# Optimization experiments

Measured on AMD Instinct MI355X. Metric: run time of the kernel, lower is better.

The kernel has to match this reference:

```python
import jax, jax.numpy as jnp
import numpy as np
from jax import lax

EPS = 1e-8

def _norm(v, eps=EPS):
    # matches torch F.normalize: v / max(||v||, eps)
    return v / jnp.maximum(jnp.linalg.norm(v, axis=-1, keepdims=True), eps)

def keep_r6(r6):
    v1 = _norm(r6[..., :3])
    v2 = r6[..., 3:6]
    v2 = v2 - jnp.sum(v2 * v1, axis=-1, keepdims=True) * v1
    v2n = jnp.linalg.norm(v2, axis=-1, keepdims=True)
    mask = (v2n < 1e-6).astype(r6.dtype)
    e1 = jnp.array([1.0, 0.0, 0.0], dtype=r6.dtype)
    e2 = jnp.array([0.0, 1.0, 0.0], dtype=r6.dtype)
    dot = jnp.abs(jnp.sum(v1 * e1, axis=-1, keepdims=True))
    fb = jnp.where(dot < 0.9, e1, e2)
    fb_v2 = jnp.cross(v1, jnp.broadcast_to(fb, v1.shape), axis=-1)
    v2 = (1.0 - mask) * v2 + mask * fb_v2
    v2 = _norm(v2)
    return jnp.concatenate([v1, v2], axis=-1)

def r6_to_matrix(r6):
    r6 = keep_r6(r6)
    v1, v2 = r6[..., :3], r6[..., 3:6]
    v3 = jnp.cross(v1, v2, axis=-1)
    R = jnp.stack([v1, v2, v3], axis=-1)  # columns v1,v2,v3
    det = jnp.linalg.det(R)
    return R * jnp.sign(det)[..., None, None]

def instance_norm(x, eps=1e-5):
    # InstanceNorm3d, affine=False: per-(B,C) stats over spatial dims, biased var
    mu = jnp.mean(x, axis=(2, 3, 4), keepdims=True)
    var = jnp.mean((x - mu) ** 2, axis=(2, 3, 4), keepdims=True)
    return (x - mu) * lax.rsqrt(var + eps)

def conv1x1(x, w, b):
    return jnp.einsum('oc,bcdhw->bodhw', w[:, :, 0, 0, 0], x) + b[None, :, None, None, None]

def conv3_circ(x, w, b):
    xp = jnp.pad(x, ((0, 0), (0, 0), (1, 1), (1, 1), (1, 1)), mode='wrap')
    out = lax.conv_general_dilated(xp, w, (1, 1, 1), 'VALID',
                                   dimension_numbers=('NCDHW', 'OIDHW', 'NCDHW'))
    return out + b[None, :, None, None, None]

def _gelu(t):
    return jax.nn.gelu(t, approximate=False)

def _forward(x, pos_emb, qkv_w, qkv_b, lp1_w, lp1_b, lp2_w, lp2_b,
             mod1_w, mod1_b, mod2_w, mod2_b, pa_w, pa_b,
             R6_d, R6_h, R6_w, proj_w, proj_b):
    B, C, D, H, W = x.shape
    NH = pa_w.shape[0]
    HD = C // NH
    NV = HD // 3
    scale = HD ** (-0.5)

    # PositionalProcessing (deterministic; computed once, reused for all 3 axes)
    local = conv1x1(_gelu(instance_norm(conv3_circ(pos_emb, lp1_w, lp1_b))), lp2_w, lp2_b)
    mod = jax.nn.sigmoid(conv1x1(_gelu(instance_norm(conv1x1(local, mod1_w, mod1_b))), mod2_w, mod2_b))
    x_mod = x * mod
    pos_attn = _gelu(instance_norm(conv1x1(pos_emb, pa_w, pa_b)))  # [B,NH,D,H,W]

    axes = [
        (R6_d, (0, 3, 4, 1, 2), (0, 4, 3, 1, 2)),  # depth
        (R6_h, (0, 2, 4, 1, 3), (0, 4, 1, 3, 2)),  # height
        (R6_w, (0, 2, 3, 1, 4), (0, 4, 1, 2, 3)),  # width
    ]
    out_sum = 0.0
    for R6, perm, inv in axes:
        xp = jnp.transpose(x_mod, perm)      # [B, A1, A2, C, L]
        Bb, A1, A2, _, L = xp.shape
        bd = Bb * A1 * A2
        xl = jnp.swapaxes(xp.reshape(bd, C, L), -1, -2)  # [bd, L, C]
        qkv = (xl @ qkv_w.T + qkv_b).reshape(bd, L, 3, NH, HD)
        qkv = jnp.transpose(qkv, (2, 0, 3, 1, 4))
        q, k, v = qkv[0], qkv[1], qkv[2]     # [bd, NH, L, HD]
        R = r6_to_matrix(keep_r6(R6))[0]     # [NH, 3, 3]

        def rot(t):
            tv = t.reshape(bd, NH, L, NV, 3)
            return jnp.einsum('hij,bhlvj->bhlvi', R, tv).reshape(bd, NH, L, HD)

        attn = jnp.einsum('bhqd,bhkd->bhqk', rot(q), rot(k)) * scale
        pa = jnp.transpose(pos_attn, perm).reshape(bd, NH, L)
        attn = jax.nn.softmax(attn + pa[..., None], axis=-1)
        o = jnp.einsum('bhqk,bhkd->bhqd', attn, v)      # [bd, NH, L, HD]
        o = jnp.swapaxes(o, 1, 2).reshape(Bb, A1, A2, L, C)
        out_sum = out_sum + jnp.transpose(o, inv)        # [B, C, D, H, W]
    return conv1x1(out_sum, proj_w, proj_b)


def setup_inputs() -> dict:
    key = jax.random.key(0)
    ks = jax.random.split(key, 20)
    B, C, D, H, W, NH = 2, 96, 40, 40, 40, 4

    def rn(k, shape, s=0.05):
        return jax.random.normal(k, shape, dtype=jnp.float32) * s

    return {
        'x': jax.random.normal(ks[0], (B, C, D, H, W), dtype=jnp.float32),
        'pos_emb': jax.random.normal(ks[1], (B, C, D, H, W), dtype=jnp.float32),
        'qkv_w': rn(ks[2], (3 * C, C)), 'qkv_b': rn(ks[3], (3 * C,)),
        'lp1_w': rn(ks[4], (C, C, 3, 3, 3)), 'lp1_b': rn(ks[5], (C,)),
        'lp2_w': rn(ks[6], (C, C, 1, 1, 1)), 'lp2_b': rn(ks[7], (C,)),
        'mod1_w': rn(ks[8], (C, C, 1, 1, 1)), 'mod1_b': rn(ks[9], (C,)),
        'mod2_w': rn(ks[10], (C, C, 1, 1, 1)), 'mod2_b': rn(ks[11], (C,)),
        'pa_w': rn(ks[12], (NH, C, 1, 1, 1)), 'pa_b': rn(ks[13], (NH,)),
        'R6_d': jax.random.normal(ks[14], (1, NH, 6), dtype=jnp.float32),
        'R6_h': jax.random.normal(ks[15], (1, NH, 6), dtype=jnp.float32),
        'R6_w': jax.random.normal(ks[16], (1, NH, 6), dtype=jnp.float32),
        'proj_w': rn(ks[17], (C, C, 1, 1, 1)), 'proj_b': rn(ks[18], (C,)),
    }


def reference(x, pos_emb, qkv_w, qkv_b, lp1_w, lp1_b, lp2_w, lp2_b,
              mod1_w, mod1_b, mod2_w, mod2_b, pa_w, pa_b,
              R6_d, R6_h, R6_w, proj_w, proj_b):
    return _forward(x, pos_emb, qkv_w, qkv_b, lp1_w, lp1_b, lp2_w, lp2_b,
                    mod1_w, mod1_b, mod2_w, mod2_b, pa_w, pa_b,
                    R6_d, R6_h, R6_w, proj_w, proj_b)
```

## Files before the change

kernel.cpp:

```cpp
#include <hip/hip_runtime.h>


typedef __attribute__((ext_vector_type(8))) short short8;
typedef __attribute__((ext_vector_type(8))) _Float16 half8;
typedef __attribute__((ext_vector_type(2))) _Float16 half2;
typedef __attribute__((ext_vector_type(16))) float floatx16;

static __device__ __forceinline__ unsigned short f2bf(float f) {
    unsigned int u = __builtin_bit_cast(unsigned int, f);
    u = u + 0x7FFFu + ((u >> 16) & 1u);
    return (unsigned short)(u >> 16);
}
static __device__ __forceinline__ half2 h2(unsigned int u) {
    return __builtin_bit_cast(half2, u);
}
static __device__ __forceinline__ float fdot2(unsigned int a, unsigned int b, float c) {
    return __builtin_amdgcn_fdot2(h2(a), h2(b), c, false);
}

__global__ __launch_bounds__(256) void k_cvt_in(const float* __restrict__ pos,
                                                unsigned short* __restrict__ in_t) {
    __shared__ unsigned short lds[64][97];
    int bid = blockIdx.x;
    int b = bid / 1000, s0 = (bid % 1000) * 64;
    int t = threadIdx.x;
    for (int i = t; i < 6144; i += 256) {
        int c = i / 64, sl = i % 64;
        lds[sl][c] = f2bf(pos[(b * 96 + c) * 64000 + s0 + sl]);
    }
    __syncthreads();
    unsigned short* outp = in_t + ((size_t)b * 64000 + s0) * 96;
    for (int i = t; i < 6144; i += 256) {
        int sl = i / 96, c = i % 96;
        outp[i] = lds[sl][c];
    }
}

__global__ void k_cvt_w(const float* __restrict__ w, unsigned short* __restrict__ wb2) {
    int i = blockIdx.x * 256 + threadIdx.x;
    if (i < 248832) {
        int c = i % 96, m = (i / 96) % 96, tap = i / 9216;
        wb2[i] = f2bf(w[(m * 96 + c) * 27 + tap]);
    }
}

__global__ void k_cvt_f16(const float* __restrict__ w, _Float16* __restrict__ o, int n) {
    int i = blockIdx.x * 256 + threadIdx.x;
    if (i < n) o[i] = (_Float16)w[i];
}

__global__ __launch_bounds__(256) void k_conv3_mfma(const unsigned short* __restrict__ in_t,
                                                    const unsigned short* __restrict__ wb2,
                                                    const float* __restrict__ bias,
                                                    float* __restrict__ out) {
    __shared__ unsigned short A_lds[96 * 104];
    __shared__ int tbl[27 * 256];
    __shared__ float bsh[96];
    int t = threadIdx.x;
    int bid = blockIdx.x;
    int b = bid / 250;
    int s0 = (bid % 250) * 256;

    for (int u = t; u < 27 * 256; u += 256) {
        int tap = u >> 8, nl = u & 255;
        int kd = tap / 9, kh = (tap / 3) % 3, kw = tap % 3;
        int s = s0 + nl;
        int d = s / 1600, r = s - d * 1600;
        int h = r / 40, w = r - h * 40;
        int ds = d + kd - 1; if (ds < 0) ds += 40; else if (ds >= 40) ds -= 40;
        int hs = h + kh - 1; if (hs < 0) hs += 40; else if (hs >= 40) hs -= 40;
        int wv2 = w + kw - 1; if (wv2 < 0) wv2 += 40; else if (wv2 >= 40) wv2 -= 40;
        tbl[u] = ((ds * 1600 + hs * 40 + wv2) * 96) * 2;
    }
    if (t < 96) bsh[t] = bias[t];

    int wv = t >> 6;
    int lane = t & 63;
    int n31 = lane & 31;
    int kg = lane >> 5;

    const char* inb = (const char*)(in_t + (size_t)b * 64000 * 96) + kg * 16;

    floatx16 acc[3][2];
#pragma unroll
    for (int mt = 0; mt < 3; mt++)
#pragma unroll
        for (int nt = 0; nt < 2; nt++)
#pragma unroll
            for (int r = 0; r < 16; r++) acc[mt][nt][r] = 0.f;

    for (int tap = 0; tap < 27; tap++) {
        __syncthreads();
        const uint4* wsrc = (const uint4*)(wb2 + tap * 9216);
        for (int u = t; u < 1152; u += 256) {
            int m = u / 12, seg = u % 12;
            uint4 v = wsrc[u];
            *(uint4*)((char*)A_lds + m * 208 + seg * 16) = v;
        }
        __syncthreads();
        int ta0 = tbl[tap * 256 + wv * 64 + n31];
        int ta1 = tbl[tap * 256 + wv * 64 + 32 + n31];
        const char* pb0 = inb + ta0;
        const char* pb1 = inb + ta1;
#pragma unroll
        for (int j = 0; j < 6; j++) {
            short8 a0 = *(short8*)((char*)A_lds + (n31) * 208 + j * 32 + kg * 16);
            short8 a1 = *(short8*)((char*)A_lds + (32 + n31) * 208 + j * 32 + kg * 16);
            short8 a2 = *(short8*)((char*)A_lds + (64 + n31) * 208 + j * 32 + kg * 16);
            short8 b0 = *(const short8*)(pb0 + j * 32);
            short8 b1 = *(const short8*)(pb1 + j * 32);
            acc[0][0] = __builtin_amdgcn_mfma_f32_32x32x16_bf16(a0, b0, acc[0][0], 0, 0, 0);
            acc[0][1] = __builtin_amdgcn_mfma_f32_32x32x16_bf16(a0, b1, acc[0][1], 0, 0, 0);
            acc[1][0] = __builtin_amdgcn_mfma_f32_32x32x16_bf16(a1, b0, acc[1][0], 0, 0, 0);
            acc[1][1] = __builtin_amdgcn_mfma_f32_32x32x16_bf16(a1, b1, acc[1][1], 0, 0, 0);
            acc[2][0] = __builtin_amdgcn_mfma_f32_32x32x16_bf16(a2, b0, acc[2][0], 0, 0, 0);
            acc[2][1] = __builtin_amdgcn_mfma_f32_32x32x16_bf16(a2, b1, acc[2][1], 0, 0, 0);
        }
    }

    int sbase = s0 + wv * 64;
#pragma unroll
    for (int mt = 0; mt < 3; mt++)
#pragma unroll
        for (int nt = 0; nt < 2; nt++)
#pragma unroll
            for (int r = 0; r < 16; r++) {
                int o = mt * 32 + (r & 3) + 8 * (r >> 2) + 4 * kg;
                int s = sbase + nt * 32 + n31;
                out[(b * 96 + o) * 64000 + s] = acc[mt][nt][r] + bsh[o];
            }
}

__global__ __launch_bounds__(256) void k_stats(const float* __restrict__ in, float2* __restrict__ stats) {
    int bc = blockIdx.x;
    const float4* p = (const float4*)(in + (size_t)bc * 64000);
    int t = threadIdx.x;
    float s = 0.f, sq = 0.f;
    for (int i = t; i < 16000; i += 256) {
        float4 v = p[i];
        s += v.x + v.y + v.z + v.w;
        sq += v.x * v.x + v.y * v.y + v.z * v.z + v.w * v.w;
    }
    __shared__ float rs[256], rq[256];
    rs[t] = s; rq[t] = sq;
    __syncthreads();
    for (int off = 128; off > 0; off >>= 1) {
        if (t < off) { rs[t] += rs[t + off]; rq[t] += rq[t + off]; }
        __syncthreads();
    }
    if (t == 0) {
        float mu = rs[0] * (1.f / 64000.f);
        float var = rq[0] * (1.f / 64000.f) - mu * mu;
        stats[bc] = make_float2(mu, rsqrtf(var + 1e-5f));
    }
}

__global__ __launch_bounds__(256) void k_norm_gelu(float* __restrict__ x, const float2* __restrict__ stats) {
    int i = blockIdx.x * 256 + threadIdx.x;
    int bc = i / 16000;
    float2 st = stats[bc];
    float4 v = ((const float4*)x)[i];
    float* f = &v.x;
#pragma unroll
    for (int q = 0; q < 4; q++) {
        float u = (f[q] - st.x) * st.y;
        f[q] = 0.5f * u * (1.f + erff(u * 0.70710678118654752f));
    }
    ((float4*)x)[i] = v;
}

__global__ __launch_bounds__(256) void k_xmod_t(const float* __restrict__ x, const float* __restrict__ m,
                                                _Float16* __restrict__ xt) {
    __shared__ _Float16 lds[64][104];
    int bid = blockIdx.x;
    int b = bid / 1000, s0 = (bid % 1000) * 64;
    int t = threadIdx.x;
    for (int i = t; i < 6144; i += 256) {
        int c = i / 64, sl = i % 64;
        int gi = (b * 96 + c) * 64000 + s0 + sl;
        lds[sl][c] = (_Float16)(x[gi] * m[gi]);
    }
    __syncthreads();
    for (int i = t; i < 768; i += 256) {
        int sl = i / 12, seg = i % 12;
        _Float16 tmp[8];
#pragma unroll
        for (int e = 0; e < 8; e++) tmp[e] = lds[sl][seg * 8 + e];
        *(uint4*)&xt[((size_t)(b * 64000 + s0 + sl)) * 96 + seg * 8] = *(uint4*)tmp;
    }
}

template <int MODE>
__global__ __launch_bounds__(256) void k_conv1x1(const float* __restrict__ in,
                                                 const float* __restrict__ w,
                                                 const float* __restrict__ bias,
                                                 float* __restrict__ out) {
    __shared__ float wl[96][98];
    __shared__ float it[96][64];
    int bid = blockIdx.x;
    int b = bid / 1000;
    int s0 = (bid % 1000) * 64;
    int t = threadIdx.x;
    for (int i = t; i < 96 * 96; i += 256) wl[i % 96][i / 96] = w[i];
    for (int i = t; i < 96 * 64; i += 256) {
        int c = i / 64, sl = i % 64;
        it[c][sl] = in[(b * 96 + c) * 64000 + s0 + sl];
    }
    __syncthreads();
    int og = t / 16, sg = t % 16;
    float acc[6][4];
#pragma unroll
    for (int j = 0; j < 6; j++)
#pragma unroll
        for (int q = 0; q < 4; q++) acc[j][q] = 0.f;
    for (int c = 0; c < 96; c++) {
        float4 v = *(const float4*)&it[c][sg * 4];
#pragma unroll
        for (int j = 0; j < 6; j++) {
            float wv = wl[c][og * 6 + j];
            acc[j][0] += wv * v.x; acc[j][1] += wv * v.y; acc[j][2] += wv * v.z; acc[j][3] += wv * v.w;
        }
    }
#pragma unroll
    for (int j = 0; j < 6; j++) {
        int o = og * 6 + j;
        float bb = bias[o];
        float4 rr;
        rr.x = acc[j][0] + bb; rr.y = acc[j][1] + bb; rr.z = acc[j][2] + bb; rr.w = acc[j][3] + bb;
        if (MODE == 1) {
            rr.x = 1.f / (1.f + expf(-rr.x)); rr.y = 1.f / (1.f + expf(-rr.y));
            rr.z = 1.f / (1.f + expf(-rr.z)); rr.w = 1.f / (1.f + expf(-rr.w));
        }
        *(float4*)&out[(b * 96 + o) * 64000 + s0 + sg * 4] = rr;
    }
}

__global__ __launch_bounds__(256) void k_qkv(const _Float16* __restrict__ xt,
                                             const _Float16* __restrict__ wq,
                                             const float* __restrict__ qb,
                                             _Float16* __restrict__ qA) {
    __shared__ _Float16 smem[27648];
    __shared__ float bias_s[288];
    int t = threadIdx.x;
    int bid = blockIdx.x;
    int b = bid / 500;
    int s0 = (bid % 500) * 128;

    for (int i = t; i < 3456; i += 256) ((uint4*)smem)[i] = ((const uint4*)wq)[i];
    for (int i = t; i < 288; i += 256) bias_s[i] = qb[i];
    __syncthreads();

    int ws = t >> 6, lane = t & 63;
    int n = lane & 31, kg = lane >> 5;
    int p = ws * 32 + n;

    const uint4* brow = (const uint4*)(xt + ((size_t)(b * 64000 + s0 + p)) * 96);
    uint4 bf[6];
#pragma unroll
    for (int kc = 0; kc < 6; kc++) bf[kc] = brow[kc * 2 + kg];

    floatx16 acc[9];
#pragma unroll
    for (int mt = 0; mt < 9; mt++)
#pragma unroll
        for (int r = 0; r < 16; r++) acc[mt][r] = 0.f;

#pragma unroll
    for (int kc = 0; kc < 6; kc++) {
        half8 bfh = __builtin_bit_cast(half8, bf[kc]);
#pragma unroll
        for (int mt = 0; mt < 9; mt++) {
            uint4 au = *(const uint4*)&smem[(mt * 32 + n) * 96 + kc * 16 + kg * 8];
            acc[mt] = __builtin_amdgcn_mfma_f32_32x32x16_f16(__builtin_bit_cast(half8, au), bfh, acc[mt], 0, 0, 0);
        }
    }

    const float scale = 0.20412414523193154f;
    for (int q = 0; q < 2; q++) {
        __syncthreads();
        if ((ws >> 1) == q) {
            int pl = (ws & 1) * 32 + n;
#pragma unroll
            for (int mt = 0; mt < 9; mt++)
#pragma unroll
                for (int g = 0; g < 4; g++) {
                    int m0 = mt * 32 + g * 8 + kg * 4;
                    _Float16 tm[4];
#pragma unroll
                    for (int j = 0; j < 4; j++) {
                        float v = acc[mt][g * 4 + j] + bias_s[m0 + j];
                        if (m0 + j < 96) v *= scale;
                        tm[j] = (_Float16)v;
                    }
                    *(uint2*)&smem[pl * 296 + m0] = *(uint2*)tm;
                }
        }
        __syncthreads();
        for (int idx = t; idx < 2304; idx += 256) {
            int pl = idx / 36, seg = idx % 36;
            int s = s0 + q * 64 + pl;
            uint4 v = *(const uint4*)&smem[pl * 296 + seg * 8];
            *(uint4*)&qA[((size_t)(b * 64000 + s)) * 288 + seg * 8] = v;
        }
    }
}

template <int AXIS>
__global__ __launch_bounds__(320, 3) void k_attn(const _Float16* __restrict__ qA,
                                                 _Float16* __restrict__ oA) {
    __shared__ _Float16 kk[8352];
    __shared__ _Float16 vT[7744];
    int t = threadIdx.x;
    int bid = blockIdx.x;
    int b = bid / 800;
    int r0 = (bid % 800) * 2;

    auto smap = [&](int r, int l) -> int {
        if (AXIS == 0) return l * 1600 + r;
        else if (AXIS == 1) { int d = r / 40, w = r % 40; return d * 1600 + l * 40 + w; }
        else return r * 40 + l;
    };
    const uint4* src = (const uint4*)qA;
    for (int i = t; i < 960; i += 320) {
        int line = i / 480, key = (i % 480) / 12, seg = i % 12;
        int row = b * 64000 + smap(r0 + line, key);
        ((uint4*)kk)[i] = src[(size_t)row * 36 + 12 + seg];
    }
    for (int i = t; i < 960; i += 320) {
        int line = i / 480, key = (i % 480) / 12, seg = i % 12;
        int row = b * 64000 + smap(r0 + line, key);
        uint4 v = src[(size_t)row * 36 + 24 + seg];
        _Float16 tmp[8];
        *(uint4*)tmp = v;
#pragma unroll
        for (int e = 0; e < 8; e++) {
            int hdg = seg * 8 + e;
            vT[(line * 4 + hdg / 24) * 968 + (hdg % 24) * 40 + key] = tmp[e];
        }
    }

    int line = t / 160, head = (t % 160) / 40, ql = t % 40;
    int rr = r0 + line;
    uint qu[12];
    {
        const uint4* qp = (const uint4*)(qA + ((size_t)(b * 64000 + smap(rr, ql))) * 288 + head * 24);
#pragma unroll
        for (int j = 0; j < 3; j++) *(uint4*)&qu[j * 4] = qp[j];
    }
    __syncthreads();

    float s[40];
    const uint4* kbase = (const uint4*)kk + line * 480 + head * 3;
#pragma unroll 4
    for (int key = 0; key < 40; key++) {
        uint kku[12];
#pragma unroll
        for (int j = 0; j < 3; j++) *(uint4*)&kku[j * 4] = kbase[key * 12 + j];
        float a = 0.f;
#pragma unroll
        for (int i = 0; i < 12; i++) a = fdot2(kku[i], qu[i], a);
        s[key] = a;
    }

    float mx = -1e30f;
#pragma unroll
    for (int i = 0; i < 40; i++) mx = fmaxf(mx, s[i]);
    float sum = 0.f;
#pragma unroll
    for (int i = 0; i < 40; i++) { s[i] = __expf(s[i] - mx); sum += s[i]; }
    float inv = 1.f / sum;

    uint pw[20];
#pragma unroll
    for (int i = 0; i < 20; i++) {
        half2 a = { (_Float16)(s[2 * i] * inv), (_Float16)(s[2 * i + 1] * inv) };
        pw[i] = __builtin_bit_cast(unsigned int, a);
    }

    __syncthreads();

    float o[24];
    const uint4* vbase = (const uint4*)vT + (line * 4 + head) * 121;
#pragma unroll 2
    for (int hd = 0; hd < 24; hd++) {
        uint vv[20];
#pragma unroll
        for (int j = 0; j < 5; j++) *(uint4*)&vv[j * 4] = vbase[hd * 5 + j];
        float a = 0.f;
#pragma unroll
        for (int i = 0; i < 20; i++) a = fdot2(vv[i], pw[i], a);
        o[hd] = a;
    }

    {
        _Float16 tm[24];
#pragma unroll
        for (int j = 0; j < 24; j++) tm[j] = (_Float16)o[j];
        _Float16* dA = &kk[(line * 40 + ql) * 104 + head * 24];
#pragma unroll
        for (int j = 0; j < 3; j++) ((uint4*)dA)[j] = ((uint4*)tm)[j];
    }
    __syncthreads();

    uint4* dst = (uint4*)oA + ((size_t)(b * 64000 + r0 * 40)) * 12;
    for (int i = t; i < 960; i += 320) {
        int row = i / 12, seg = i % 12;
        dst[i] = *(const uint4*)&kk[row * 104 + seg * 8];
    }
}

__global__ __launch_bounds__(256) void k_proj(const _Float16* __restrict__ o0,
                                              const _Float16* __restrict__ o1,
                                              const _Float16* __restrict__ o2,
                                              const _Float16* __restrict__ wp,
                                              const float* __restrict__ pb,
                                              float* __restrict__ out) {
    __shared__ _Float16 A[9216];
    __shared__ float bias_s[96];
    int t = threadIdx.x;
    int bid = blockIdx.x;
    int b = bid / 500;
    int s0 = (bid % 500) * 128;
    for (int i = t; i < 1152; i += 256) ((uint4*)A)[i] = ((const uint4*)wp)[i];
    if (t < 96) bias_s[t] = pb[t];
    __syncthreads();

    int ws = t >> 6, lane = t & 63;
    int n = lane & 31, kg = lane >> 5;
    int s = s0 + ws * 32 + n;

    int l0 = s / 1600, r0v = s % 1600;
    int row0 = r0v * 40 + l0;
    int d = s / 1600, rem = s % 1600, lh = rem / 40, wq2 = rem % 40;
    int row1 = (d * 40 + wq2) * 40 + lh;
    int row2 = s;

    const uint4* p0 = (const uint4*)(o0 + ((size_t)(b * 64000 + row0)) * 96);
    const uint4* p1 = (const uint4*)(o1 + ((size_t)(b * 64000 + row1)) * 96);
    const uint4* p2 = (const uint4*)(o2 + ((size_t)(b * 64000 + row2)) * 96);

    uint4 bf[3][6];
#pragma unroll
    for (int kc = 0; kc < 6; kc++) {
        bf[0][kc] = p0[kc * 2 + kg];
        bf[1][kc] = p1[kc * 2 + kg];
        bf[2][kc] = p2[kc * 2 + kg];
    }

    floatx16 acc[3];
#pragma unroll
    for (int mt = 0; mt < 3; mt++)
#pragma unroll
        for (int r = 0; r < 16; r++) acc[mt][r] = 0.f;

#pragma unroll
    for (int kc = 0; kc < 6; kc++) {
#pragma unroll
        for (int mt = 0; mt < 3; mt++) {
            uint4 au = *(const uint4*)&A[(mt * 32 + n) * 96 + kc * 16 + kg * 8];
            half8 ah = __builtin_bit_cast(half8, au);
            acc[mt] = __builtin_amdgcn_mfma_f32_32x32x16_f16(ah, __builtin_bit_cast(half8, bf[0][kc]), acc[mt], 0, 0, 0);
            acc[mt] = __builtin_amdgcn_mfma_f32_32x32x16_f16(ah, __builtin_bit_cast(half8, bf[1][kc]), acc[mt], 0, 0, 0);
            acc[mt] = __builtin_amdgcn_mfma_f32_32x32x16_f16(ah, __builtin_bit_cast(half8, bf[2][kc]), acc[mt], 0, 0, 0);
        }
    }

#pragma unroll
    for (int mt = 0; mt < 3; mt++)
#pragma unroll
        for (int r = 0; r < 16; r++) {
            int m = mt * 32 + (r & 3) + 8 * (r >> 2) + 4 * kg;
            out[((size_t)(b * 96 + m)) * 64000 + s] = acc[mt][r] + bias_s[m];
        }
}

extern "C" void kernel_launch(void* const* d_in, const int* in_sizes, int n_in,
                              void* d_out, int out_size, void* d_ws, size_t ws_size,
                              hipStream_t stream) {
    const float* x      = (const float*)d_in[0];
    const float* pos    = (const float*)d_in[1];
    const float* qkv_w  = (const float*)d_in[2];
    const float* qkv_b  = (const float*)d_in[3];
    const float* lp1_w  = (const float*)d_in[4];
    const float* lp1_b  = (const float*)d_in[5];
    const float* lp2_w  = (const float*)d_in[6];
    const float* lp2_b  = (const float*)d_in[7];
    const float* mod1_w = (const float*)d_in[8];
    const float* mod1_b = (const float*)d_in[9];
    const float* mod2_w = (const float*)d_in[10];
    const float* mod2_b = (const float*)d_in[11];
    const float* proj_w = (const float*)d_in[17];
    const float* proj_b = (const float*)d_in[18];
    float* out = (float*)d_out;
    float* ws = (float*)d_ws;

    float* buf0 = ws;
    float* buf1 = ws + 12288000;
    float2* stats = (float2*)(ws + 24576000);
    unsigned short* wb2 = (unsigned short*)(ws + 24576384);
    _Float16* wq  = (_Float16*)(ws + 24700800);
    _Float16* wpj = (_Float16*)(ws + 24714624);
    _Float16* qA  = (_Float16*)(ws + 24720000);
    unsigned short* in_t = (unsigned short*)buf1;
    _Float16* x_t = (_Float16*)buf0;
    _Float16* o2  = (_Float16*)(buf0 + 6144000);
    _Float16* o0  = (_Float16*)buf1;
    _Float16* o1  = (_Float16*)buf1 + 12288000;

    k_cvt_in<<<2000, 256, 0, stream>>>(pos, in_t);
    k_cvt_w<<<972, 256, 0, stream>>>(lp1_w, wb2);
    k_cvt_f16<<<108, 256, 0, stream>>>(qkv_w, wq, 27648);
    k_cvt_f16<<<36, 256, 0, stream>>>(proj_w, wpj, 9216);

    k_conv3_mfma<<<500, 256, 0, stream>>>(in_t, wb2, lp1_b, buf0);
    k_stats<<<192, 256, 0, stream>>>(buf0, stats);
    k_norm_gelu<<<12000, 256, 0, stream>>>(buf0, stats);
    k_conv1x1<0><<<2000, 256, 0, stream>>>(buf0, lp2_w, lp2_b, buf1);

    k_conv1x1<0><<<2000, 256, 0, stream>>>(buf1, mod1_w, mod1_b, buf0);
    k_stats<<<192, 256, 0, stream>>>(buf0, stats);
    k_norm_gelu<<<12000, 256, 0, stream>>>(buf0, stats);
    k_conv1x1<1><<<2000, 256, 0, stream>>>(buf0, mod2_w, mod2_b, buf1);

    k_xmod_t<<<2000, 256, 0, stream>>>(x, buf1, x_t);

    k_qkv<<<1000, 256, 0, stream>>>(x_t, wq, qkv_b, qA);
    k_attn<0><<<1600, 320, 0, stream>>>(qA, o0);
    k_attn<1><<<1600, 320, 0, stream>>>(qA, o1);
    k_attn<2><<<1600, 320, 0, stream>>>(qA, o2);

    k_proj<<<1000, 256, 0, stream>>>(o0, o1, o2, wpj, proj_b, out);
}
```

Baseline: 748.8 us.

## Restructure positional pipeline in fp16 channel-last with folded 1x1 convs and accumulated attention

Switches the conv3 path from bf16 to fp16 and reads weights directly from global memory instead of staging per tap in LDS. Intermediates are now stored as fp16 channel-last rather than fp32 channel-first, which roughly halves traffic. The lp2 and mod1 1x1 convs are folded algebraically into one weight since no nonlinearity sits between them. Stats become a split reduction with atomics, the x*mod product is fused into the sigmoid GEMM epilogue, and the three attention outputs are summed in place so proj runs one GEMM instead of three. Risks include fp16 overflow or precision loss and non-deterministic atomic accumulation.

Result: faster. 677.4 us (-9.5%).

```diff
diff --git a/kernel.cpp b/kernel.cpp
--- a/kernel.cpp
+++ b/kernel.cpp
@@ -1,16 +1,10 @@
 #include <hip/hip_runtime.h>
 
 
-typedef __attribute__((ext_vector_type(8))) short short8;
 typedef __attribute__((ext_vector_type(8))) _Float16 half8;
 typedef __attribute__((ext_vector_type(2))) _Float16 half2;
 typedef __attribute__((ext_vector_type(16))) float floatx16;
 
-static __device__ __forceinline__ unsigned short f2bf(float f) {
-    unsigned int u = __builtin_bit_cast(unsigned int, f);
-    u = u + 0x7FFFu + ((u >> 16) & 1u);
-    return (unsigned short)(u >> 16);
-}
 static __device__ __forceinline__ half2 h2(unsigned int u) {
     return __builtin_bit_cast(half2, u);
 }
@@ -18,29 +12,34 @@
     return __builtin_amdgcn_fdot2(h2(a), h2(b), c, false);
 }
 
+__global__ void k_zero(float* __restrict__ p) {
+    int t = threadIdx.x;
+    for (int i = t; i < 768; i += 256) p[i] = 0.f;
+}
+
 __global__ __launch_bounds__(256) void k_cvt_in(const float* __restrict__ pos,
-                                                unsigned short* __restrict__ in_t) {
-    __shared__ unsigned short lds[64][97];
+                                                _Float16* __restrict__ in_t) {
+    __shared__ _Float16 lds[64][97];
     int bid = blockIdx.x;
     int b = bid / 1000, s0 = (bid % 1000) * 64;
     int t = threadIdx.x;
     for (int i = t; i < 6144; i += 256) {
         int c = i / 64, sl = i % 64;
-        lds[sl][c] = f2bf(pos[(b * 96 + c) * 64000 + s0 + sl]);
-    }
-    __syncthreads();
-    unsigned short* outp = in_t + ((size_t)b * 64000 + s0) * 96;
+        lds[sl][c] = (_Float16)pos[(b * 96 + c) * 64000 + s0 + sl];
+    }
+    __syncthreads();
+    _Float16* outp = in_t + ((size_t)b * 64000 + s0) * 96;
     for (int i = t; i < 6144; i += 256) {
         int sl = i / 96, c = i % 96;
         outp[i] = lds[sl][c];
     }
 }
 
-__global__ void k_cvt_w(const float* __restrict__ w, unsigned short* __restrict__ wb2) {
+__global__ void k_cvt_w(const float* __restrict__ w, _Float16* __restrict__ wf) {
     int i = blockIdx.x * 256 + threadIdx.x;
     if (i < 248832) {
         int c = i % 96, m = (i / 96) % 96, tap = i / 9216;
-        wb2[i] = f2bf(w[(m * 96 + c) * 27 + tap]);
+        wf[i] = (_Float16)w[(m * 96 + c) * 27 + tap];
     }
 }
 
@@ -49,12 +48,33 @@
     if (i < n) o[i] = (_Float16)w[i];
 }
 
-__global__ __launch_bounds__(256) void k_conv3_mfma(const unsigned short* __restrict__ in_t,
-                                                    const unsigned short* __restrict__ wb2,
-                                                    const float* __restrict__ bias,
-                                                    float* __restrict__ out) {
-    __shared__ unsigned short A_lds[96 * 104];
+__global__ __launch_bounds__(256) void k_fold(const float* __restrict__ lp2_w,
+                                              const float* __restrict__ lp2_b,
+                                              const float* __restrict__ mod1_w,
+                                              const float* __restrict__ mod1_b,
+                                              _Float16* __restrict__ wfold,
+                                              float* __restrict__ bfold) {
+    int i = blockIdx.x * 256 + threadIdx.x;
+    if (i < 9216) {
+        int o = i / 96, c = i % 96;
+        float a = 0.f;
+        for (int k = 0; k < 96; k++) a += mod1_w[o * 96 + k] * lp2_w[k * 96 + c];
+        wfold[i] = (_Float16)a;
+    }
+    if (blockIdx.x == 0 && threadIdx.x < 96) {
+        int o = threadIdx.x;
+        float a = mod1_b[o];
+        for (int k = 0; k < 96; k++) a += mod1_w[o * 96 + k] * lp2_b[k];
+        bfold[o] = a;
+    }
+}
+
+__global__ __launch_bounds__(256) void k_conv3_v2(const _Float16* __restrict__ in_t,
+                                                  const _Float16* __restrict__ wf,
+                                                  const float* __restrict__ bias,
+                                                  _Float16* __restrict__ c3) {
     __shared__ int tbl[27 * 256];
+    __shared__ _Float16 st[256 * 98];
     __shared__ float bsh[96];
     int t = threadIdx.x;
     int bid = blockIdx.x;
@@ -73,12 +93,10 @@
         tbl[u] = ((ds * 1600 + hs * 40 + wv2) * 96) * 2;
     }
     if (t < 96) bsh[t] = bias[t];
-
-    int wv = t >> 6;
-    int lane = t & 63;
-    int n31 = lane & 31;
-    int kg = lane >> 5;
-
+    __syncthreads();
+
+    int wv = t >> 6, lane = t & 63;
+    int n31 = lane & 31, kg = lane >> 5;
     const char* inb = (const char*)(in_t + (size_t)b * 64000 * 96) + kg * 16;
 
     floatx16 acc[3][2];
@@ -90,148 +108,164 @@
             for (int r = 0; r < 16; r++) acc[mt][nt][r] = 0.f;
 
     for (int tap = 0; tap < 27; tap++) {
-        __syncthreads();
-        const uint4* wsrc = (const uint4*)(wb2 + tap * 9216);
-        for (int u = t; u < 1152; u += 256) {
-            int m = u / 12, seg = u % 12;
-            uint4 v = wsrc[u];
-            *(uint4*)((char*)A_lds + m * 208 + seg * 16) = v;
-        }
-        __syncthreads();
         int ta0 = tbl[tap * 256 + wv * 64 + n31];
         int ta1 = tbl[tap * 256 + wv * 64 + 32 + n31];
         const char* pb0 = inb + ta0;
         const char* pb1 = inb + ta1;
+        const _Float16* wt = wf + tap * 9216 + kg * 8;
 #pragma unroll
         for (int j = 0; j < 6; j++) {
-            short8 a0 = *(short8*)((char*)A_lds + (n31) * 208 + j * 32 + kg * 16);
-            short8 a1 = *(short8*)((char*)A_lds + (32 + n31) * 208 + j * 32 + kg * 16);
-            short8 a2 = *(short8*)((char*)A_lds + (64 + n31) * 208 + j * 32 + kg * 16);
-            short8 b0 = *(const short8*)(pb0 + j * 32);
-            short8 b1 = *(const short8*)(pb1 + j * 32);
-            acc[0][0] = __builtin_amdgcn_mfma_f32_32x32x16_bf16(a0, b0, acc[0][0], 0, 0, 0);
-            acc[0][1] = __builtin_amdgcn_mfma_f32_32x32x16_bf16(a0, b1, acc[0][1], 0, 0, 0);
-            acc[1][0] = __builtin_amdgcn_mfma_f32_32x32x16_bf16(a1, b0, acc[1][0], 0, 0, 0);
-            acc[1][1] = __builtin_amdgcn_mfma_f32_32x32x16_bf16(a1, b1, acc[1][1], 0, 0, 0);
-            acc[2][0] = __builtin_amdgcn_mfma_f32_32x32x16_bf16(a2, b0, acc[2][0], 0, 0, 0);
-            acc[2][1] = __builtin_amdgcn_mfma_f32_32x32x16_bf16(a2, b1, acc[2][1], 0, 0, 0);
-        }
-    }
-
-    int sbase = s0 + wv * 64;
+            half8 a0 = *(const half8*)(wt + (n31) * 96 + j * 16);
+            half8 a1 = *(const half8*)(wt + (32 + n31) * 96 + j * 16);
+            half8 a2 = *(const half8*)(wt + (64 + n31) * 96 + j * 16);
+            half8 b0 = *(const half8*)(pb0 + j * 32);
+            half8 b1 = *(const half8*)(pb1 + j * 32);
+            acc[0][0] = __builtin_amdgcn_mfma_f32_32x32x16_f16(a0, b0, acc[0][0], 0, 0, 0);
+            acc[0][1] = __builtin_amdgcn_mfma_f32_32x32x16_f16(a0, b1, acc[0][1], 0, 0, 0);
+            acc[1][0] = __builtin_amdgcn_mfma_f32_32x32x16_f16(a1, b0, acc[1][0], 0, 0, 0);
+            acc[1][1] = __builtin_amdgcn_mfma_f32_32x32x16_f16(a1, b1, acc[1][1], 0, 0, 0);
+            acc[2][0] = __builtin_amdgcn_mfma_f32_32x32x16_f16(a2, b0, acc[2][0], 0, 0, 0);
+            acc[2][1] = __builtin_amdgcn_mfma_f32_32x32x16_f16(a2, b1, acc[2][1], 0, 0, 0);
+        }
+    }
+
 #pragma unroll
     for (int mt = 0; mt < 3; mt++)
 #pragma unroll
         for (int nt = 0; nt < 2; nt++)
 #pragma unroll
             for (int r = 0; r < 16; r++) {
-                int o = mt * 32 + (r & 3) + 8 * (r >> 2) + 4 * kg;
-                int s = sbase + nt * 32 + n31;
-                out[(b * 96 + o) * 64000 + s] = acc[mt][nt][r] + bsh[o];
+                int m = mt * 32 + (r & 3) + 8 * (r >> 2) + 4 * kg;
+                int sl = wv * 64 + nt * 32 + n31;
+                st[sl * 98 + m] = (_Float16)(acc[mt][nt][r] + bsh[m]);
             }
-}
-
-__global__ __launch_bounds__(256) void k_stats(const float* __restrict__ in, float2* __restrict__ stats) {
-    int bc = blockIdx.x;
-    const float4* p = (const float4*)(in + (size_t)bc * 64000);
-    int t = threadIdx.x;
-    float s = 0.f, sq = 0.f;
-    for (int i = t; i < 16000; i += 256) {
-        float4 v = p[i];
-        s += v.x + v.y + v.z + v.w;
-        sq += v.x * v.x + v.y * v.y + v.z * v.z + v.w * v.w;
-    }
-    __shared__ float rs[256], rq[256];
-    rs[t] = s; rq[t] = sq;
-    __syncthreads();
-    for (int off = 128; off > 0; off >>= 1) {
-        if (t < off) { rs[t] += rs[t + off]; rq[t] += rq[t + off]; }
-        __syncthreads();
-    }
-    if (t == 0) {
-        float mu = rs[0] * (1.f / 64000.f);
-        float var = rq[0] * (1.f / 64000.f) - mu * mu;
-        stats[bc] = make_float2(mu, rsqrtf(var + 1e-5f));
-    }
-}
-
-__global__ __launch_bounds__(256) void k_norm_gelu(float* __restrict__ x, const float2* __restrict__ stats) {
-    int i = blockIdx.x * 256 + threadIdx.x;
-    int bc = i / 16000;
-    float2 st = stats[bc];
-    float4 v = ((const float4*)x)[i];
-    float* f = &v.x;
-#pragma unroll
-    for (int q = 0; q < 4; q++) {
-        float u = (f[q] - st.x) * st.y;
-        f[q] = 0.5f * u * (1.f + erff(u * 0.70710678118654752f));
-    }
-    ((float4*)x)[i] = v;
-}
-
-__global__ __launch_bounds__(256) void k_xmod_t(const float* __restrict__ x, const float* __restrict__ m,
-                                                _Float16* __restrict__ xt) {
-    __shared__ _Float16 lds[64][104];
+    __syncthreads();
+
+    unsigned int* dst = (unsigned int*)(c3 + ((size_t)(b * 64000 + s0)) * 96);
+    for (int i = t; i < 12288; i += 256) {
+        int row = i / 48, sg = i % 48;
+        dst[i] = *(const unsigned int*)&st[row * 98 + sg * 2];
+    }
+}
+
+__global__ __launch_bounds__(192) void k_stats_sc(const _Float16* __restrict__ in,
+                                                  float* __restrict__ raw) {
+    __shared__ float red_s[16][96], red_q[16][96];
     int bid = blockIdx.x;
-    int b = bid / 1000, s0 = (bid % 1000) * 64;
-    int t = threadIdx.x;
+    int b = bid / 50, ch = bid % 50;
+    int t = threadIdx.x;
+    int sp = t / 12, cs = t % 12;
+    const uint4* base = (const uint4*)(in + ((size_t)(b * 64000 + ch * 1280)) * 96);
+    float s8[8], q8[8];
+#pragma unroll
+    for (int e = 0; e < 8; e++) { s8[e] = 0.f; q8[e] = 0.f; }
+    for (int i = 0; i < 80; i++) {
+        uint4 v = base[(sp + i * 16) * 12 + cs];
+        half8 h = __builtin_bit_cast(half8, v);
+#pragma unroll
+        for (int e = 0; e < 8; e++) { float f = (float)h[e]; s8[e] += f; q8[e] += f * f; }
+    }
+#pragma unroll
+    for (int e = 0; e < 8; e++) { red_s[sp][cs * 8 + e] = s8[e]; red_q[sp][cs * 8 + e] = q8[e]; }
+    __syncthreads();
+    if (t < 96) {
+        float S = 0.f, Q = 0.f;
+        for (int k = 0; k < 16; k++) { S += red_s[k][t]; Q += red_q[k][t]; }
+        atomicAdd(&raw[(b * 96 + t) * 2], S);
+        atomicAdd(&raw[(b * 96 + t) * 2 + 1], Q);
+    }
+}
+
+__global__ void k_finalize(const float* __restrict__ raw, float2* __restrict__ sf) {
+    int t = threadIdx.x;
+    if (t < 192) {
+        float S = raw[t * 2], Q = raw[t * 2 + 1];
+        float mu = S * (1.f / 64000.f);
+        float var = Q * (1.f / 64000.f) - mu * mu;
+        sf[t] = make_float2(mu, rsqrtf(var + 1e-5f));
+    }
+}
+
+__global__ __launch_bounds__(256) void k_ng16(_Float16* __restrict__ x, const float2* __restrict__ sf) {
+    int t = threadIdx.x, bid = blockIdx.x;
+    uint4* p = (uint4*)x;
+#pragma unroll
+    for (int k = 0; k < 4; k++) {
+        int i = bid * 1024 + k * 256 + t;
+        int e0 = i * 8;
+        int b = e0 / 6144000;
+        int c0 = e0 % 96;
+        const float2* sp = &sf[b * 96 + c0];
+        uint4 v = p[i];
+        half8 h = __builtin_bit_cast(half8, v);
+        _Float16 o[8];
+#pragma unroll
+        for (int e = 0; e < 8; e++) {
+            float2 st = sp[e];
+            float u = ((float)h[e] - st.x) * st.y;
+            o[e] = (_Float16)(0.5f * u * (1.f + erff(u * 0.70710678118654752f)));
+        }
+        p[i] = *(uint4*)o;
+    }
+}
+
+template <int MODE>
+__global__ __launch_bounds__(256) void k_gemm96(const _Float16* __restrict__ in,
+                                                const _Float16* __restrict__ w,
+                                                const float* __restrict__ bias,
+                                                const float* __restrict__ xg,
+                                                _Float16* __restrict__ outp) {
+    __shared__ _Float16 un[12544];
+    __shared__ float bias_s[96];
+    int t = threadIdx.x, bid = blockIdx.x;
+    int b = bid / 500, s0 = (bid % 500) * 128;
+    for (int i = t; i < 1152; i += 256) ((uint4*)un)[i] = ((const uint4*)w)[i];
+    if (t < 96) bias_s[t] = bias[t];
+    __syncthreads();
+
+    int ws = t >> 6, lane = t & 63;
+    int n = lane & 31, kg = lane >> 5;
+    int p = ws * 32 + n;
+    const uint4* brow = (const uint4*)(in + ((size_t)(b * 64000 + s0 + p)) * 96);
+    uint4 bf[6];
+#pragma unroll
+    for (int kc = 0; kc < 6; kc++) bf[kc] = brow[kc * 2 + kg];
+
+    floatx16 acc[3];
+#pragma unroll
+    for (int mt = 0; mt < 3; mt++)
+#pragma unroll
+        for (int r = 0; r < 16; r++) acc[mt][r] = 0.f;
+#pragma unroll
+    for (int kc = 0; kc < 6; kc++) {
+        half8 bfh = __builtin_bit_cast(half8, bf[kc]);
+#pragma unroll
+        for (int mt = 0; mt < 3; mt++) {
+            uint4 au = *(const uint4*)&un[(mt * 32 + n) * 96 + kc * 16 + kg * 8];
+            acc[mt] = __builtin_amdgcn_mfma_f32_32x32x16_f16(__builtin_bit_cast(half8, au), bfh, acc[mt], 0, 0, 0);
+        }
+    }
+    __syncthreads();
+
+#pragma unroll
+    for (int mt = 0; mt < 3; mt++)
+#pragma unroll
+        for (int r = 0; r < 16; r++) {
+            int m = mt * 32 + (r & 3) + 8 * (r >> 2) + 4 * kg;
+            int sl = ws * 32 + n;
+            float v = acc[mt][r] + bias_s[m];
+            if (MODE == 1) {
+                v = 1.f / (1.f + __expf(-v));
+                v *= xg[((size_t)(b * 96 + m)) * 64000 + s0 + sl];
+            }
+            un[sl * 98 + m] = (_Float16)v;
+        }
+    __syncthreads();
+
+    unsigned int* dst = (unsigned int*)(outp + ((size_t)(b * 64000 + s0)) * 96);
     for (int i = t; i < 6144; i += 256) {
-        int c = i / 64, sl = i % 64;
-        int gi = (b * 96 + c) * 64000 + s0 + sl;
-        lds[sl][c] = (_Float16)(x[gi] * m[gi]);
-    }
-    __syncthreads();
-    for (int i = t; i < 768; i += 256) {
-        int sl = i / 12, seg = i % 12;
-        _Float16 tmp[8];
-#pragma unroll
-        for (int e = 0; e < 8; e++) tmp[e] = lds[sl][seg * 8 + e];
-        *(uint4*)&xt[((size_t)(b * 64000 + s0 + sl)) * 96 + seg * 8] = *(uint4*)tmp;
-    }
-}
-
-template <int MODE>
-__global__ __launch_bounds__(256) void k_conv1x1(const float* __restrict__ in,
-                                                 const float* __restrict__ w,
-                                                 const float* __restrict__ bias,
-                                                 float* __restrict__ out) {
-    __shared__ float wl[96][98];
-    __shared__ float it[96][64];
-    int bid = blockIdx.x;
-    int b = bid / 1000;
-    int s0 = (bid % 1000) * 64;
-    int t = threadIdx.x;
-    for (int i = t; i < 96 * 96; i += 256) wl[i % 96][i / 96] = w[i];
-    for (int i = t; i < 96 * 64; i += 256) {
-        int c = i / 64, sl = i % 64;
-        it[c][sl] = in[(b * 96 + c) * 64000 + s0 + sl];
-    }
-    __syncthreads();
-    int og = t / 16, sg = t % 16;
-    float acc[6][4];
-#pragma unroll
-    for (int j = 0; j < 6; j++)
-#pragma unroll
-        for (int q = 0; q < 4; q++) acc[j][q] = 0.f;
-    for (int c = 0; c < 96; c++) {
-        float4 v = *(const float4*)&it[c][sg * 4];
-#pragma unroll
-        for (int j = 0; j < 6; j++) {
-            float wv = wl[c][og * 6 + j];
-            acc[j][0] += wv * v.x; acc[j][1] += wv * v.y; acc[j][2] += wv * v.z; acc[j][3] += wv * v.w;
-        }
-    }
-#pragma unroll
-    for (int j = 0; j < 6; j++) {
-        int o = og * 6 + j;
-        float bb = bias[o];
-        float4 rr;
-        rr.x = acc[j][0] + bb; rr.y = acc[j][1] + bb; rr.z = acc[j][2] + bb; rr.w = acc[j][3] + bb;
-        if (MODE == 1) {
-            rr.x = 1.f / (1.f + expf(-rr.x)); rr.y = 1.f / (1.f + expf(-rr.y));
-            rr.z = 1.f / (1.f + expf(-rr.z)); rr.w = 1.f / (1.f + expf(-rr.w));
-        }
-        *(float4*)&out[(b * 96 + o) * 64000 + s0 + sg * 4] = rr;
+        int row = i / 48, sg = i % 48;
+        dst[i] = *(const unsigned int*)&un[row * 98 + sg * 2];
     }
 }
 
@@ -305,9 +339,9 @@
     }
 }
 
-template <int AXIS>
+template <int AXIS, bool ACC>
 __global__ __launch_bounds__(320, 3) void k_attn(const _Float16* __restrict__ qA,
-                                                 _Float16* __restrict__ oA) {
+                                                 _Float16* __restrict__ osum) {
     __shared__ _Float16 kk[8352];
     __shared__ _Float16 vT[7744];
     int t = threadIdx.x;
@@ -341,7 +375,7 @@
 
     int line = t / 160, head = (t % 160) / 40, ql = t % 40;
     int rr = r0 + line;
-    uint qu[12];
+    unsigned int qu[12];
     {
         const uint4* qp = (const uint4*)(qA + ((size_t)(b * 64000 + smap(rr, ql))) * 288 + head * 24);
 #pragma unroll
@@ -353,7 +387,7 @@
     const uint4* kbase = (const uint4*)kk + line * 480 + head * 3;
 #pragma unroll 4
     for (int key = 0; key < 40; key++) {
-        uint kku[12];
+        unsigned int kku[12];
 #pragma unroll
         for (int j = 0; j < 3; j++) *(uint4*)&kku[j * 4] = kbase[key * 12 + j];
         float a = 0.f;
@@ -370,7 +404,7 @@
     for (int i = 0; i < 40; i++) { s[i] = __expf(s[i] - mx); sum += s[i]; }
     float inv = 1.f / sum;
 
-    uint pw[20];
+    unsigned int pw[20];
 #pragma unroll
     for (int i = 0; i < 20; i++) {
         half2 a = { (_Float16)(s[2 * i] * inv), (_Float16)(s[2 * i + 1] * inv) };
@@ -383,7 +417,7 @@
     const uint4* vbase = (const uint4*)vT + (line * 4 + head) * 121;
 #pragma unroll 2
     for (int hd = 0; hd < 24; hd++) {
-        uint vv[20];
+        unsigned int vv[20];
 #pragma unroll
         for (int j = 0; j < 5; j++) *(uint4*)&vv[j * 4] = vbase[hd * 5 + j];
         float a = 0.f;
@@ -402,16 +436,23 @@
     }
     __syncthreads();
 
-    uint4* dst = (uint4*)oA + ((size_t)(b * 64000 + r0 * 40)) * 12;
+    uint4* dst = (uint4*)osum;
     for (int i = t; i < 960; i += 320) {
         int row = i / 12, seg = i % 12;
-        dst[i] = *(const uint4*)&kk[row * 104 + seg * 8];
-    }
-}
-
-__global__ __launch_bounds__(256) void k_proj(const _Float16* __restrict__ o0,
-                                              const _Float16* __restrict__ o1,
-                                              const _Float16* __restrict__ o2,
+        int s2 = smap(r0 + row / 40, row % 40);
+        size_t di = ((size_t)(b * 64000 + s2)) * 12 + seg;
+        uint4 v = *(const uint4*)&kk[row * 104 + seg * 8];
+        if (ACC) {
+            half8 a = __builtin_bit_cast(half8, dst[di]);
+            half8 c = __builtin_bit_cast(half8, v);
+            dst[di] = __builtin_bit_cast(uint4, a + c);
+        } else {
+            dst[di] = v;
+        }
+    }
+}
+
+__global__ __launch_bounds__(256) void k_proj(const _Float16* __restrict__ osum,
                                               const _Float16* __restrict__ wp,
                                               const float* __restrict__ pb,
                                               float* __restrict__ out) {
@@ -429,39 +470,24 @@
     int n = lane & 31, kg = lane >> 5;
     int s = s0 + ws * 32 + n;
 
-    int l0 = s / 1600, r0v = s % 1600;
-    int row0 = r0v * 40 + l0;
-    int d = s / 1600, rem = s % 1600, lh = rem / 40, wq2 = rem % 40;
-    int row1 = (d * 40 + wq2) * 40 + lh;
-    int row2 = s;
-
-    const uint4* p0 = (const uint4*)(o0 + ((size_t)(b * 64000 + row0)) * 96);
-    const uint4* p1 = (const uint4*)(o1 + ((size_t)(b * 64000 + row1)) * 96);
-    const uint4* p2 = (const uint4*)(o2 + ((size_t)(b * 64000 + row2)) * 96);
-
-    uint4 bf[3][6];
+    const uint4* brow = (const uint4*)(osum + ((size_t)(b * 64000 + s0 + ws * 32 + n)) * 96);
+    uint4 bf[6];
+#pragma unroll
+    for (int kc = 0; kc < 6; kc++) bf[kc] = brow[kc * 2 + kg];
+
+    floatx16 acc[3];
+#pragma unroll
+    for (int mt = 0; mt < 3; mt++)
+#pragma unroll
+        for (int r = 0; r < 16; r++) acc[mt][r] = 0.f;
+
 #pragma unroll
     for (int kc = 0; kc < 6; kc++) {
-        bf[0][kc] = p0[kc * 2 + kg];
-        bf[1][kc] = p1[kc * 2 + kg];
-        bf[2][kc] = p2[kc * 2 + kg];
-    }
-
-    floatx16 acc[3];
-#pragma unroll
-    for (int mt = 0; mt < 3; mt++)
-#pragma unroll
-        for (int r = 0; r < 16; r++) acc[mt][r] = 0.f;
-
-#pragma unroll
-    for (int kc = 0; kc < 6; kc++) {
+        half8 bfh = __builtin_bit_cast(half8, bf[kc]);
 #pragma unroll
         for (int mt = 0; mt < 3; mt++) {
             uint4 au = *(const uint4*)&A[(mt * 32 + n) * 96 + kc * 16 + kg * 8];
-            half8 ah = __builtin_bit_cast(half8, au);
-            acc[mt] = __builtin_amdgcn_mfma_f32_32x32x16_f16(ah, __builtin_bit_cast(half8, bf[0][kc]), acc[mt], 0, 0, 0);
-            acc[mt] = __builtin_amdgcn_mfma_f32_32x32x16_f16(ah, __builtin_bit_cast(half8, bf[1][kc]), acc[mt], 0, 0, 0);
-            acc[mt] = __builtin_amdgcn_mfma_f32_32x32x16_f16(ah, __builtin_bit_cast(half8, bf[2][kc]), acc[mt], 0, 0, 0);
+            acc[mt] = __builtin_amdgcn_mfma_f32_32x32x16_f16(__builtin_bit_cast(half8, au), bfh, acc[mt], 0, 0, 0);
         }
     }
 
@@ -494,40 +520,43 @@
     float* out = (float*)d_out;
     float* ws = (float*)d_ws;
 
-    float* buf0 = ws;
-    float* buf1 = ws + 12288000;
-    float2* stats = (float2*)(ws + 24576000);
-    unsigned short* wb2 = (unsigned short*)(ws + 24576384);
-    _Float16* wq  = (_Float16*)(ws + 24700800);
-    _Float16* wpj = (_Float16*)(ws + 24714624);
-    _Float16* qA  = (_Float16*)(ws + 24720000);
-    unsigned short* in_t = (unsigned short*)buf1;
-    _Float16* x_t = (_Float16*)buf0;
-    _Float16* o2  = (_Float16*)(buf0 + 6144000);
-    _Float16* o0  = (_Float16*)buf1;
-    _Float16* o1  = (_Float16*)buf1 + 12288000;
-
+    _Float16* bufA = (_Float16*)ws;
+    _Float16* bufB = (_Float16*)(ws + 6144000);
+    _Float16* qA   = (_Float16*)(ws + 12288000);
+    _Float16* in_t = qA;
+    _Float16* wf   = (_Float16*)(ws + 30720000);
+    _Float16* wq   = (_Float16*)(ws + 30844416);
+    _Float16* wpj  = (_Float16*)(ws + 30858240);
+    _Float16* wfold= (_Float16*)(ws + 30862848);
+    _Float16* wm2  = (_Float16*)(ws + 30867456);
+    float* bfold   = ws + 30872064;
+    float* raw     = ws + 30872160;
+    float2* sf0    = (float2*)(ws + 30872928);
+    float2* sf1    = (float2*)(ws + 30873312);
+    float* raw0 = raw, *raw1 = raw + 384;
+
+    k_zero<<<1, 256, 0, stream>>>(raw);
     k_cvt_in<<<2000, 256, 0, stream>>>(pos, in_t);
-    k_cvt_w<<<972, 256, 0, stream>>>(lp1_w, wb2);
+    k_cvt_w<<<972, 256, 0, stream>>>(lp1_w, wf);
+    k_fold<<<36, 256, 0, stream>>>(lp2_w, lp2_b, mod1_w, mod1_b, wfold, bfold);
+    k_cvt_f16<<<36, 256, 0, stream>>>(mod2_w, wm2, 9216);
     k_cvt_f16<<<108, 256, 0, stream>>>(qkv_w, wq, 27648);
     k_cvt_f16<<<36, 256, 0, stream>>>(proj_w, wpj, 9216);
 
-    k_conv3_mfma<<<500, 256, 0, stream>>>(in_t, wb2, lp1_b, buf0);
-    k_stats<<<192, 256, 0, stream>>>(buf0, stats);
-    k_norm_gelu<<<12000, 256, 0, stream>>>(buf0, stats);
-    k_conv1x1<0><<<2000, 256, 0, stream>>>(buf0, lp2_w, lp2_b, buf1);
-
-    k_conv1x1<0><<<2000, 256, 0, stream>>>(buf1, mod1_w, mod1_b, buf0);
-    k_stats<<<192, 256, 0, stream>>>(buf0, stats);
-    k_norm_gelu<<<12000, 256, 0, stream>>>(buf0, stats);
-    k_conv1x1<1><<<2000, 256, 0, stream>>>(buf0, mod2_w, mod2_b, buf1);
-
-    k_xmod_t<<<2000, 256, 0, stream>>>(x, buf1, x_t);
-
-    k_qkv<<<1000, 256, 0, stream>>>(x_t, wq, qkv_b, qA);
-    k_attn<0><<<1600, 320, 0, stream>>>(qA, o0);
-    k_attn<1><<<1600, 320, 0, stream>>>(qA, o1);
-    k_attn<2><<<1600, 320, 0, stream>>>(qA, o2);
-
-    k_proj<<<1000, 256, 0, stream>>>(o0, o1, o2, wpj, proj_b, out);
-}
+    k_conv3_v2<<<500, 256, 0, stream>>>(in_t, wf, lp1_b, bufA);
+    k_stats_sc<<<100, 192, 0, stream>>>(bufA, raw0);
+    k_finalize<<<1, 256, 0, stream>>>(raw0, sf0);
+    k_ng16<<<1500, 256, 0, stream>>>(bufA, sf0);
+    k_gemm96<0><<<1000, 256, 0, stream>>>(bufA, wfold, bfold, nullptr, bufB);
+    k_stats_sc<<<100, 192, 0, stream>>>(bufB, raw1);
+    k_finalize<<<1, 256, 0, stream>>>(raw1, sf1);
+    k_ng16<<<1500, 256, 0, stream>>>(bufB, sf1);
+    k_gemm96<1><<<1000, 256, 0, stream>>>(bufB, wm2, mod2_b, x, bufA);
+
+    k_qkv<<<1000, 256, 0, stream>>>(bufA, wq, qkv_b, qA);
+    k_attn<2, false><<<1600, 320, 0, stream>>>(qA, bufB);
+    k_attn<0, true ><<<1600, 320, 0, stream>>>(qA, bufB);
+    k_attn<1, true ><<<1600, 320, 0, stream>>>(qA, bufB);
+
+    k_proj<<<1000, 256, 0, stream>>>(bufB, wpj, proj_b, out);
+}
```
